# Performance work log

Measured on AMD Instinct MI355X. Metric: run time of the kernel, lower is better.

The kernel has to match this reference:

```python
import jax, jax.numpy as jnp
import numpy as np

B, S, D, H, MLP = 2, 2048, 1024, 16, 4096
DH = D // H
EPS_LN = 1e-6
KERNEL_EPS = 1e-3  # fast_attention generalized kernel_epsilon


def layer_norm(x, scale, bias):
    m = jnp.mean(x, axis=-1, keepdims=True)
    v = jnp.mean(jnp.square(x - m), axis=-1, keepdims=True)
    return (x - m) * jax.lax.rsqrt(v + EPS_LN) * scale + bias


def performer_causal_attention(q, k, v):
    """FAVOR+ generalized attention (deterministic relu features), causal.

    q,k,v: [B,S,H,DH]. phi(x) = relu(x) + eps. Linear-time via prefix sums:
      out_i = phi(q_i) . cumsum_j<=i phi(k_j) v_j^T / (phi(q_i) . cumsum phi(k_j))
    """
    phi_q = jax.nn.relu(q) + KERNEL_EPS          # [B,S,H,M]
    phi_k = jax.nn.relu(k) + KERNEL_EPS          # [B,S,H,M]
    kv = jnp.cumsum(jnp.einsum('bshm,bshd->bshmd', phi_k, v), axis=1)  # [B,S,H,M,DH]
    num = jnp.einsum('bshm,bshmd->bshd', phi_q, kv)
    den = jnp.einsum('bshm,bshm->bsh', phi_q, jnp.cumsum(phi_k, axis=1))
    return num / den[..., None]


def setup_inputs() -> dict:
    key = jax.random.key(0)
    ks = jax.random.split(key, 7)
    def w(k, shape, scale):
        return jax.random.normal(k, shape, jnp.float32) * scale
    s_in = 1.0 / np.sqrt(D)
    return {
        'inputs': jax.random.normal(ks[0], (B, S, D), jnp.float32),
        'ln1_scale': jnp.ones((D,), jnp.float32),
        'ln1_bias': jnp.zeros((D,), jnp.float32),
        'wq': w(ks[1], (D, H, DH), s_in),
        'wk': w(ks[2], (D, H, DH), s_in),
        'wv': w(ks[3], (D, H, DH), s_in),
        'wo': w(ks[4], (H, DH, D), s_in),
        'ln2_scale': jnp.ones((D,), jnp.float32),
        'ln2_bias': jnp.zeros((D,), jnp.float32),
        'w1': w(ks[5], (D, MLP), s_in),
        'b1': jnp.zeros((MLP,), jnp.float32),
        'w2': w(ks[6], (MLP, D), 1.0 / np.sqrt(MLP)),
        'b2': jnp.zeros((D,), jnp.float32),
    }


def reference(inputs, ln1_scale, ln1_bias, wq, wk, wv, wo,
              ln2_scale, ln2_bias, w1, b1, w2, b2):
    # pre-LN self-attention (Performer FAVOR+ generalized, causal)
    x = layer_norm(inputs, ln1_scale, ln1_bias)
    q = jnp.einsum('bsd,dhm->bshm', x, wq)
    k = jnp.einsum('bsd,dhm->bshm', x, wk)
    v = jnp.einsum('bsd,dhm->bshm', x, wv)
    attn = performer_causal_attention(q, k, v)          # [B,S,H,DH]
    attn_out = jnp.einsum('bshm,hmd->bsd', attn, wo)    # output projection
    x = attn_out + inputs                               # residual
    # pre-LN MLP block
    y = layer_norm(x, ln2_scale, ln2_bias)
    y = jax.nn.gelu(y @ w1 + b1) @ w2 + b2
    return x + y
```

## Files before the change

### kernel.cpp

```cpp
#include <hip/hip_runtime.h>
#include <math.h>
#include <stdint.h>

typedef __bf16 bf16;
typedef bf16  bf16x8 __attribute__((ext_vector_type(8)));
typedef float f32x4  __attribute__((ext_vector_type(4)));

constexpr int Bb  = 2;
constexpr int Ss  = 2048;
constexpr int Dd  = 1024;
constexpr int Hh  = 16;
constexpr int DHh = 64;
constexpr int MLPd = 4096;
constexpr int ROWS = Bb * Ss;
constexpr int NC  = Ss / 64;
constexpr int BH  = Bb * Hh;
constexpr float EPS_LN = 1e-6f;
constexpr float KEPS   = 1e-3f;

__device__ __forceinline__ void async_copy16(const bf16* g, bf16* l) {
    __builtin_amdgcn_global_load_lds(
        (__attribute__((address_space(1))) void*)g,
        (__attribute__((address_space(3))) void*)l,
        16, 0, 0);
}

__device__ __forceinline__ int swz64(int row, int col) {
    return row * 64 + (((col >> 3) ^ row) & 7) * 8 + (col & 7);
}

__global__ __launch_bounds__(256) void ln_kernel(const float* __restrict__ x,
                                                 const float* __restrict__ scale,
                                                 const float* __restrict__ bias,
                                                 bf16* __restrict__ out)
{
    const int row = blockIdx.x;
    const float* xr = x + (size_t)row * Dd;
    float vals[4];
    float sum = 0.f, sumsq = 0.f;
#pragma unroll
    for (int i = 0; i < 4; i++) {
        float v = xr[threadIdx.x + 256 * i];
        vals[i] = v;
        sum += v;
        sumsq += v * v;
    }
#pragma unroll
    for (int off = 32; off > 0; off >>= 1) {
        sum   += __shfl_down(sum, off);
        sumsq += __shfl_down(sumsq, off);
    }
    __shared__ float ssum[4], ssq[4];
    const int wave = threadIdx.x >> 6;
    if ((threadIdx.x & 63) == 0) { ssum[wave] = sum; ssq[wave] = sumsq; }
    __syncthreads();
    const float tot   = ssum[0] + ssum[1] + ssum[2] + ssum[3];
    const float totsq = ssq[0] + ssq[1] + ssq[2] + ssq[3];
    const float mean = tot * (1.f / Dd);
    const float var  = totsq * (1.f / Dd) - mean * mean;
    const float r = rsqrtf(var + EPS_LN);
    bf16* orow = out + (size_t)row * Dd;
#pragma unroll
    for (int i = 0; i < 4; i++) {
        const int c = threadIdx.x + 256 * i;
        orow[c] = (bf16)((vals[i] - mean) * r * scale[c] + bias[c]);
    }
}

__global__ __launch_bounds__(256) void convert_T(const float* __restrict__ in,
                                                 bf16* __restrict__ out,
                                                 int K, int N)
{
    __shared__ float tile[32][33];
    const int k0 = blockIdx.y * 32, n0 = blockIdx.x * 32;
    const int tx = threadIdx.x & 31, ty = threadIdx.x >> 5;
#pragma unroll
    for (int i = 0; i < 32; i += 8)
        tile[ty + i][tx] = in[(size_t)(k0 + ty + i) * N + n0 + tx];
    __syncthreads();
#pragma unroll
    for (int i = 0; i < 32; i += 8)
        out[(size_t)(n0 + ty + i) * K + k0 + tx] = (bf16)tile[tx][ty + i];
}

__global__ __launch_bounds__(256) void convert_T4(const float* __restrict__ s0,
                                                  const float* __restrict__ s1,
                                                  const float* __restrict__ s2,
                                                  const float* __restrict__ s3,
                                                  bf16* __restrict__ d0,
                                                  bf16* __restrict__ d1,
                                                  bf16* __restrict__ d2,
                                                  bf16* __restrict__ d3)
{
    const float* in  = (blockIdx.z == 0) ? s0 : (blockIdx.z == 1) ? s1
                     : (blockIdx.z == 2) ? s2 : s3;
    bf16* out        = (blockIdx.z == 0) ? d0 : (blockIdx.z == 1) ? d1
                     : (blockIdx.z == 2) ? d2 : d3;
    __shared__ float tile[32][33];
    const int k0 = blockIdx.y * 32, n0 = blockIdx.x * 32;
    const int tx = threadIdx.x & 31, ty = threadIdx.x >> 5;
#pragma unroll
    for (int i = 0; i < 32; i += 8)
        tile[ty + i][tx] = in[(size_t)(k0 + ty + i) * 1024 + n0 + tx];
    __syncthreads();
#pragma unroll
    for (int i = 0; i < 32; i += 8)
        out[(size_t)(n0 + ty + i) * 1024 + k0 + tx] = (bf16)tile[tx][ty + i];
}

enum { EP_QKV = 0, EP_NONE = 1, EP_RES = 2, EP_GELU = 3, EP_BIAS_RES = 4 };

template <int TN, int BK, int MODE>
__global__ __launch_bounds__(256) void mfma_gemm(const bf16* __restrict__ A,
                                                 const bf16* __restrict__ BT,
                                                 void* __restrict__ Cout,
                                                 int M, int N, int K,
                                                 const float* __restrict__ bias,
                                                 const float* __restrict__ res,
                                                 bf16* __restrict__ out2,
                                                 bf16* __restrict__ out3)
{
    constexpr int WCT = TN / 2;
    constexpr int NJ  = TN / 32;
    constexpr int NS  = BK / 32;
    constexpr int CPR = BK / 8;
    constexpr int RPI = 2048 / BK;
    __shared__ bf16 As[128 * BK];
    __shared__ bf16 Bs[TN * BK];
    const int t = threadIdx.x;
    const int wave = t >> 6, lane = t & 63;
    const int row0 = blockIdx.y * 128, col0 = blockIdx.x * TN;
    const int wr = wave >> 1, wc = wave & 1;

    const int srow = t / CPR;
    const int gch  = (t % CPR) ^ (srow & 7);
    const int sdst = t * 8;

    const int m = lane & 15, quad = lane >> 4;
    const int mx7 = m & 7;

    f32x4 acc[4][NJ] = {};

    for (int k0 = 0; k0 < K; k0 += BK) {
        __syncthreads();
#pragma unroll
        for (int i = 0; i < 128 / RPI; i++) {
            const int r = i * RPI + srow;
            async_copy16(A + (size_t)(row0 + r) * K + k0 + gch * 8,
                         &As[i * 2048 + sdst]);
        }
#pragma unroll
        for (int i = 0; i < TN / RPI; i++) {
            const int r = i * RPI + srow;
            async_copy16(BT + (size_t)(col0 + r) * K + k0 + gch * 8,
                         &Bs[i * 2048 + sdst]);
        }
        __syncthreads();

#pragma unroll
        for (int s = 0; s < NS; s++) {
            const int pco = ((s * 4 + quad) ^ mx7) * 8;
            bf16x8 aF[4], bF[NJ];
#pragma unroll
            for (int i = 0; i < 4; i++)
                aF[i] = *(const bf16x8*)&As[(wr * 64 + i * 16 + m) * BK + pco];
#pragma unroll
            for (int j = 0; j < NJ; j++)
                bF[j] = *(const bf16x8*)&Bs[(wc * WCT + j * 16 + m) * BK + pco];
#pragma unroll
            for (int i = 0; i < 4; i++)
#pragma unroll
                for (int j = 0; j < NJ; j++)
                    acc[i][j] = __builtin_amdgcn_mfma_f32_16x16x32_bf16(
                        aF[i], bF[j], acc[i][j], 0, 0, 0);
        }
    }

    bf16* qkv_dst = nullptr;
    int col_base = col0;
    bool do_phi = false;
    if constexpr (MODE == EP_QKV) {
        const int third = col0 >> 10;
        qkv_dst = (third == 0) ? (bf16*)Cout : (third == 1) ? out2 : out3;
        col_base = col0 & 1023;
        do_phi = (third < 2);
    }

#pragma unroll
    for (int i = 0; i < 4; i++) {
#pragma unroll
        for (int j = 0; j < NJ; j++) {
#pragma unroll
            for (int r = 0; r < 4; r++) {
                const int row = row0 + wr * 64 + i * 16 + quad * 4 + r;
                const int col = col0 + wc * WCT + j * 16 + m;
                float val = acc[i][j][r];
                if constexpr (MODE == EP_QKV) {
                    const int lc = col_base + wc * WCT + j * 16 + m;
                    if (do_phi) val = fmaxf(val, 0.f) + KEPS;
                    qkv_dst[(size_t)row * 1024 + lc] = (bf16)val;
                } else if constexpr (MODE == EP_NONE) {
                    ((bf16*)Cout)[(size_t)row * N + col] = (bf16)val;
                } else if constexpr (MODE == EP_RES) {
                    ((float*)Cout)[(size_t)row * N + col] = val + res[(size_t)row * N + col];
                } else if constexpr (MODE == EP_GELU) {
                    val += bias[col];
                    const float u = 0.7978845608028654f * (val + 0.044715f * val * val * val);
                    const float e = __expf(2.f * u);
                    val = val * (1.f - 1.f / (e + 1.f));
                    ((bf16*)Cout)[(size_t)row * N + col] = (bf16)val;
                } else {
                    val += bias[col] + res[(size_t)row * N + col];
                    ((float*)Cout)[(size_t)row * N + col] = val;
                }
            }
        }
    }
}

__global__ __launch_bounds__(256) void chunk_kv_kernel(const bf16* __restrict__ phik,
                                                       const bf16* __restrict__ v,
                                                       float* __restrict__ kvs,
                                                       float* __restrict__ ksums)
{
    const int c = blockIdx.x, bh = blockIdx.y;
    const int b = bh >> 4, h = bh & 15;
    __shared__ bf16 Kt[64 * 64];
    __shared__ bf16 Vt[64 * 64];
    const int t = threadIdx.x;
    const int wave = t >> 6, lane = t & 63;
    const int m16 = lane & 15, quad = lane >> 4;
    const int wr = wave >> 1, wc = wave & 1;
    const int f = t & 63, s4 = t >> 6;

#pragma unroll
    for (int i = 0; i < 16; i++) {
        const int s = s4 + 4 * i;
        const size_t g = ((size_t)((b * Ss + c * 64 + s) * Hh + h)) * DHh + f;
        Kt[swz64(f, s)] = phik[g];
        Vt[swz64(f, s)] = v[g];
    }
    __syncthreads();

    f32x4 acc[2][2] = {};
#pragma unroll
    for (int ks = 0; ks < 2; ks++) {
        bf16x8 aF[2], bF[2];
#pragma unroll
        for (int i = 0; i < 2; i++)
            aF[i] = *(const bf16x8*)&Kt[swz64(wr * 32 + i * 16 + m16, ks * 32 + quad * 8)];
#pragma unroll
        for (int j = 0; j < 2; j++)
            bF[j] = *(const bf16x8*)&Vt[swz64(wc * 32 + j * 16 + m16, ks * 32 + quad * 8)];
#pragma unroll
        for (int i = 0; i < 2; i++)
#pragma unroll
            for (int j = 0; j < 2; j++)
                acc[i][j] = __builtin_amdgcn_mfma_f32_16x16x32_bf16(
                    aF[i], bF[j], acc[i][j], 0, 0, 0);
    }

    const size_t base = ((size_t)bh * NC + c) * 4096;
#pragma unroll
    for (int i = 0; i < 2; i++)
#pragma unroll
        for (int j = 0; j < 2; j++)
#pragma unroll
            for (int r = 0; r < 4; r++) {
                const int mrow = wr * 32 + i * 16 + quad * 4 + r;
                const int dcol = wc * 32 + j * 16 + m16;
                kvs[base + mrow * 64 + dcol] = acc[i][j][r];
            }

    if (t < 64) {
        float s_ = 0.f;
#pragma unroll
        for (int p = 0; p < 8; p++) {
            bf16x8 k8 = *(const bf16x8*)&Kt[t * 64 + p * 8];
#pragma unroll
            for (int e = 0; e < 8; e++) s_ += (float)k8[e];
        }
        ksums[((size_t)bh * NC + c) * 64 + t] = s_;
    }
}

__global__ __launch_bounds__(256) void scan_kernel(float* __restrict__ kvs,
                                                   float* __restrict__ ksums)
{
    const int e  = blockIdx.x * 256 + threadIdx.x;
    const int bh = blockIdx.y;
    float run = 0.f;
#pragma unroll 4
    for (int c = 0; c < NC; c++) {
        const size_t idx = ((size_t)bh * NC + c) * 4096 + e;
        const float val = kvs[idx];
        kvs[idx] = run;
        run += val;
    }
    if (blockIdx.x == 0 && threadIdx.x < 64) {
        float r = 0.f;
        for (int c = 0; c < NC; c++) {
            const size_t idx = ((size_t)bh * NC + c) * 64 + threadIdx.x;
            const float val = ksums[idx];
            ksums[idx] = r;
            r += val;
        }
    }
}

__global__ __launch_bounds__(256) void attn_out_kernel(const bf16* __restrict__ phiq,
                                                       const bf16* __restrict__ phik,
                                                       const bf16* __restrict__ v,
                                                       const float* __restrict__ kvs,
                                                       const float* __restrict__ ksums,
                                                       bf16* __restrict__ attn)
{
    const int c = blockIdx.x, bh = blockIdx.y;
    const int b = bh >> 4, h = bh & 15;
    __shared__ bf16 Qs [64 * 64];
    __shared__ bf16 KVb[64 * 64];
    __shared__ bf16 Sm [64 * 64];
    __shared__ bf16 KVt[64 * 64];
    __shared__ float ksm[64], den[64];
    const int t = threadIdx.x;
    const int wave = t >> 6, lane = t & 63;
    const int m16 = lane & 15, quad = lane >> 4;
    const int wr = wave >> 1, wc = wave & 1;
    const int f = t & 63, s4 = t >> 6;

#pragma unroll
    for (int i = 0; i < 16; i++) {
        const int s = s4 + 4 * i;
        const size_t g = ((size_t)((b * Ss + c * 64 + s) * Hh + h)) * DHh + f;
        Qs [swz64(s, f)] = phiq[g];
        KVb[swz64(s, f)] = phik[g];
    }
    if (t < 64) ksm[t] = ksums[((size_t)bh * NC + c) * 64 + t];
    __syncthreads();

    f32x4 sacc[2][2] = {};
#pragma unroll
    for (int ks = 0; ks < 2; ks++) {
        bf16x8 aF[2], bF[2];
#pragma unroll
        for (int i = 0; i < 2; i++)
            aF[i] = *(const bf16x8*)&Qs [swz64(wr * 32 + i * 16 + m16, ks * 32 + quad * 8)];
#pragma unroll
        for (int j = 0; j < 2; j++)
            bF[j] = *(const bf16x8*)&KVb[swz64(wc * 32 + j * 16 + m16, ks * 32 + quad * 8)];
#pragma unroll
        for (int i = 0; i < 2; i++)
#pragma unroll
            for (int j = 0; j < 2; j++)
                sacc[i][j] = __builtin_amdgcn_mfma_f32_16x16x32_bf16(
                    aF[i], bF[j], sacc[i][j], 0, 0, 0);
    }
#pragma unroll
    for (int i = 0; i < 2; i++)
#pragma unroll
        for (int j = 0; j < 2; j++)
#pragma unroll
            for (int r = 0; r < 4; r++) {
                const int row = wr * 32 + i * 16 + quad * 4 + r;
                const int col = wc * 32 + j * 16 + m16;
                Sm[swz64(row, col)] = (bf16)((col <= row) ? sacc[i][j][r] : 0.f);
            }
    __syncthreads();

#pragma unroll
    for (int i = 0; i < 16; i++) {
        const int s = s4 + 4 * i;
        const size_t g = ((size_t)((b * Ss + c * 64 + s) * Hh + h)) * DHh + f;
        KVb[swz64(f, s)] = v[g];
    }
    {
        const size_t base = ((size_t)bh * NC + c) * 4096;
#pragma unroll
        for (int i = 0; i < 16; i++) {
            const int e = t + 256 * i;
            KVt[swz64(e & 63, e >> 6)] = (bf16)kvs[base + e];
        }
    }
    __syncthreads();

    if (t < 64) {
        float d_ = 0.f;
#pragma unroll
        for (int p = 0; p < 8; p++) {
            const int gc = (p ^ (t & 7)) * 8;
            bf16x8 q8 = *(const bf16x8*)&Qs[t * 64 + p * 8];
            bf16x8 s8 = *(const bf16x8*)&Sm[t * 64 + p * 8];
#pragma unroll
            for (int e = 0; e < 8; e++)
                d_ += (float)q8[e] * ksm[gc + e] + (float)s8[e];
        }
        den[t] = d_;
    }

    f32x4 oacc[2][2] = {};
#pragma unroll
    for (int ks = 0; ks < 2; ks++) {
        bf16x8 aF[2], bF[2];
#pragma unroll
        for (int i = 0; i < 2; i++)
            aF[i] = *(const bf16x8*)&Sm [swz64(wr * 32 + i * 16 + m16, ks * 32 + quad * 8)];
#pragma unroll
        for (int j = 0; j < 2; j++)
            bF[j] = *(const bf16x8*)&KVb[swz64(wc * 32 + j * 16 + m16, ks * 32 + quad * 8)];
#pragma unroll
        for (int i = 0; i < 2; i++)
#pragma unroll
            for (int j = 0; j < 2; j++)
                oacc[i][j] = __builtin_amdgcn_mfma_f32_16x16x32_bf16(
                    aF[i], bF[j], oacc[i][j], 0, 0, 0);
    }
#pragma unroll
    for (int ks = 0; ks < 2; ks++) {
        bf16x8 aF[2], bF[2];
#pragma unroll
        for (int i = 0; i < 2; i++)
            aF[i] = *(const bf16x8*)&Qs [swz64(wr * 32 + i * 16 + m16, ks * 32 + quad * 8)];
#pragma unroll
        for (int j = 0; j < 2; j++)
            bF[j] = *(const bf16x8*)&KVt[swz64(wc * 32 + j * 16 + m16, ks * 32 + quad * 8)];
#pragma unroll
        for (int i = 0; i < 2; i++)
#pragma unroll
            for (int j = 0; j < 2; j++)
                oacc[i][j] = __builtin_amdgcn_mfma_f32_16x16x32_bf16(
                    aF[i], bF[j], oacc[i][j], 0, 0, 0);
    }
    __syncthreads();

#pragma unroll
    for (int i = 0; i < 2; i++) {
#pragma unroll
        for (int r = 0; r < 4; r++) {
            const int row = wr * 32 + i * 16 + quad * 4 + r;
            const float dinv = 1.f / den[row];
#pragma unroll
            for (int j = 0; j < 2; j++) {
                const int col = wc * 32 + j * 16 + m16;
                attn[((size_t)((b * Ss + c * 64 + row) * Hh + h)) * DHh + col] =
                    (bf16)(oacc[i][j][r] * dinv);
            }
        }
    }
}

extern "C" void kernel_launch(void* const* d_in, const int* in_sizes, int n_in,
                              void* d_out, int out_size, void* d_ws, size_t ws_size,
                              hipStream_t stream)
{
    const float* inputs    = (const float*)d_in[0];
    const float* ln1_scale = (const float*)d_in[1];
    const float* ln1_bias  = (const float*)d_in[2];
    const float* wq        = (const float*)d_in[3];
    const float* wk        = (const float*)d_in[4];
    const float* wv        = (const float*)d_in[5];
    const float* wo        = (const float*)d_in[6];
    const float* ln2_scale = (const float*)d_in[7];
    const float* ln2_bias  = (const float*)d_in[8];
    const float* w1        = (const float*)d_in[9];
    const float* b1        = (const float*)d_in[10];
    const float* w2        = (const float*)d_in[11];
    const float* b2        = (const float*)d_in[12];
    float* out = (float*)d_out;

    char* ws = (char*)d_ws;
    bf16*  xln   = (bf16*)ws;
    bf16*  q     = (bf16*)(ws + (8ull  << 20));
    bf16*  k     = (bf16*)(ws + (16ull << 20));
    bf16*  v     = (bf16*)(ws + (24ull << 20));
    float* kvs   = (float*)(ws + (32ull << 20));
    float* x2    = (float*)(ws + (48ull << 20));
    float* ksums = (float*)(ws + (64ull << 20));
    bf16*  wqT   = (bf16*)(ws + (64ull << 20) + (1ull << 18));
    bf16*  wkT   = wqT + 1024 * 1024;
    bf16*  wvT   = wkT + 1024 * 1024;
    bf16*  woT   = wvT + 1024 * 1024;
    bf16*  w1T   = woT + 1024 * 1024;
    bf16*  w2T   = w1T + 4096 * 1024;
    bf16*  attn  = xln;
    bf16*  yln   = q;
    bf16*  hbuf  = k;

    convert_T4<<<dim3(32, 32, 4), 256, 0, stream>>>(wq, wk, wv, wo, wqT, wkT, wvT, woT);
    convert_T<<<dim3(4096 / 32, 1024 / 32), 256, 0, stream>>>(w1, w1T, 1024, 4096);
    convert_T<<<dim3(1024 / 32, 4096 / 32), 256, 0, stream>>>(w2, w2T, 4096, 1024);

    ln_kernel<<<ROWS, 256, 0, stream>>>(inputs, ln1_scale, ln1_bias, xln);

    mfma_gemm<128, 64, EP_QKV><<<dim3(3072 / 128, ROWS / 128), 256, 0, stream>>>(
        xln, wqT, q, ROWS, 3072, 1024, nullptr, nullptr, k, v);

    {
        dim3 gridA(NC, BH);
        chunk_kv_kernel<<<gridA, 256, 0, stream>>>(k, v, kvs, ksums);
        scan_kernel<<<dim3(4096 / 256, BH), 256, 0, stream>>>(kvs, ksums);
        attn_out_kernel<<<gridA, 256, 0, stream>>>(q, k, v, kvs, ksums, attn);
    }

    mfma_gemm<64, 128, EP_RES><<<dim3(1024 / 64, ROWS / 128), 256, 0, stream>>>(
        attn, woT, x2, ROWS, 1024, 1024, nullptr, inputs, nullptr, nullptr);

    ln_kernel<<<ROWS, 256, 0, stream>>>(x2, ln2_scale, ln2_bias, yln);

    mfma_gemm<128, 64, EP_GELU><<<dim3(MLPd / 128, ROWS / 128), 256, 0, stream>>>(
        yln, w1T, hbuf, ROWS, MLPd, 1024, b1, nullptr, nullptr, nullptr);
    mfma_gemm<64, 128, EP_BIAS_RES><<<dim3(1024 / 64, ROWS / 128), 256, 0, stream>>>(
        hbuf, w2T, out, ROWS, 1024, MLPd, b2, x2, nullptr, nullptr);
}
```

Baseline: 310.3 us.

## Specialize GEMM dims at compile time and store chunk KV states in bf16

The GEMM kernel now takes N and K as template parameters and advances precomputed global pointers each K step, which cuts per-iteration address arithmetic. Separately, the per-chunk KV state buffer moves from fp32 to bf16, halving traffic in chunk_kv, scan and attn_out. The scan still accumulates in fp32, but it writes bf16 prefixes, so precision is reduced slightly.

```diff
diff --git a/kernel.cpp b/kernel.cpp
--- a/kernel.cpp
+++ b/kernel.cpp
@@ -110,11 +110,10 @@
 
 enum { EP_QKV = 0, EP_NONE = 1, EP_RES = 2, EP_GELU = 3, EP_BIAS_RES = 4 };
 
-template <int TN, int BK, int MODE>
+template <int TN, int BK, int NDIM, int KDIM, int MODE>
 __global__ __launch_bounds__(256) void mfma_gemm(const bf16* __restrict__ A,
                                                  const bf16* __restrict__ BT,
                                                  void* __restrict__ Cout,
-                                                 int M, int N, int K,
                                                  const float* __restrict__ bias,
                                                  const float* __restrict__ res,
                                                  bf16* __restrict__ out2,
@@ -136,25 +135,22 @@
     const int gch  = (t % CPR) ^ (srow & 7);
     const int sdst = t * 8;
 
+    const bf16* gA = A  + (size_t)(row0 + srow) * KDIM + gch * 8;
+    const bf16* gB = BT + (size_t)(col0 + srow) * KDIM + gch * 8;
+
     const int m = lane & 15, quad = lane >> 4;
     const int mx7 = m & 7;
 
     f32x4 acc[4][NJ] = {};
 
-    for (int k0 = 0; k0 < K; k0 += BK) {
+    for (int k0 = 0; k0 < KDIM; k0 += BK) {
         __syncthreads();
 #pragma unroll
-        for (int i = 0; i < 128 / RPI; i++) {
-            const int r = i * RPI + srow;
-            async_copy16(A + (size_t)(row0 + r) * K + k0 + gch * 8,
-                         &As[i * 2048 + sdst]);
-        }
-#pragma unroll
-        for (int i = 0; i < TN / RPI; i++) {
-            const int r = i * RPI + srow;
-            async_copy16(BT + (size_t)(col0 + r) * K + k0 + gch * 8,
-                         &Bs[i * 2048 + sdst]);
-        }
+        for (int i = 0; i < 128 / RPI; i++)
+            async_copy16(gA + (size_t)i * RPI * KDIM, &As[i * 2048 + sdst]);
+#pragma unroll
+        for (int i = 0; i < TN / RPI; i++)
+            async_copy16(gB + (size_t)i * RPI * KDIM, &Bs[i * 2048 + sdst]);
         __syncthreads();
 
 #pragma unroll
@@ -174,6 +170,8 @@
                     acc[i][j] = __builtin_amdgcn_mfma_f32_16x16x32_bf16(
                         aF[i], bF[j], acc[i][j], 0, 0, 0);
         }
+        gA += BK;
+        gB += BK;
     }
 
     bf16* qkv_dst = nullptr;
@@ -200,18 +198,18 @@
                     if (do_phi) val = fmaxf(val, 0.f) + KEPS;
                     qkv_dst[(size_t)row * 1024 + lc] = (bf16)val;
                 } else if constexpr (MODE == EP_NONE) {
-                    ((bf16*)Cout)[(size_t)row * N + col] = (bf16)val;
+                    ((bf16*)Cout)[(size_t)row * NDIM + col] = (bf16)val;
                 } else if constexpr (MODE == EP_RES) {
-                    ((float*)Cout)[(size_t)row * N + col] = val + res[(size_t)row * N + col];
+                    ((float*)Cout)[(size_t)row * NDIM + col] = val + res[(size_t)row * NDIM + col];
                 } else if constexpr (MODE == EP_GELU) {
                     val += bias[col];
                     const float u = 0.7978845608028654f * (val + 0.044715f * val * val * val);
                     const float e = __expf(2.f * u);
                     val = val * (1.f - 1.f / (e + 1.f));
-                    ((bf16*)Cout)[(size_t)row * N + col] = (bf16)val;
+                    ((bf16*)Cout)[(size_t)row * NDIM + col] = (bf16)val;
                 } else {
-                    val += bias[col] + res[(size_t)row * N + col];
-                    ((float*)Cout)[(size_t)row * N + col] = val;
+                    val += bias[col] + res[(size_t)row * NDIM + col];
+                    ((float*)Cout)[(size_t)row * NDIM + col] = val;
                 }
             }
         }
@@ -220,7 +218,7 @@
 
 __global__ __launch_bounds__(256) void chunk_kv_kernel(const bf16* __restrict__ phik,
                                                        const bf16* __restrict__ v,
-                                                       float* __restrict__ kvs,
+                                                       bf16* __restrict__ kvs,
                                                        float* __restrict__ ksums)
 {
     const int c = blockIdx.x, bh = blockIdx.y;
@@ -269,7 +267,7 @@
             for (int r = 0; r < 4; r++) {
                 const int mrow = wr * 32 + i * 16 + quad * 4 + r;
                 const int dcol = wc * 32 + j * 16 + m16;
-                kvs[base + mrow * 64 + dcol] = acc[i][j][r];
+                kvs[base + mrow * 64 + dcol] = (bf16)acc[i][j][r];
             }
 
     if (t < 64) {
@@ -284,7 +282,7 @@
     }
 }
 
-__global__ __launch_bounds__(256) void scan_kernel(float* __restrict__ kvs,
+__global__ __launch_bounds__(256) void scan_kernel(bf16* __restrict__ kvs,
                                                    float* __restrict__ ksums)
 {
     const int e  = blockIdx.x * 256 + threadIdx.x;
@@ -293,8 +291,8 @@
 #pragma unroll 4
     for (int c = 0; c < NC; c++) {
         const size_t idx = ((size_t)bh * NC + c) * 4096 + e;
-        const float val = kvs[idx];
-        kvs[idx] = run;
+        const float val = (float)kvs[idx];
+        kvs[idx] = (bf16)run;
         run += val;
     }
     if (blockIdx.x == 0 && threadIdx.x < 64) {
@@ -311,7 +309,7 @@
 __global__ __launch_bounds__(256) void attn_out_kernel(const bf16* __restrict__ phiq,
                                                        const bf16* __restrict__ phik,
                                                        const bf16* __restrict__ v,
-                                                       const float* __restrict__ kvs,
+                                                       const bf16* __restrict__ kvs,
                                                        const float* __restrict__ ksums,
                                                        bf16* __restrict__ attn)
 {
@@ -378,7 +376,7 @@
 #pragma unroll
         for (int i = 0; i < 16; i++) {
             const int e = t + 256 * i;
-            KVt[swz64(e & 63, e >> 6)] = (bf16)kvs[base + e];
+            KVt[swz64(e & 63, e >> 6)] = kvs[base + e];
         }
     }
     __syncthreads();
@@ -472,7 +470,7 @@
     bf16*  q     = (bf16*)(ws + (8ull  << 20));
     bf16*  k     = (bf16*)(ws + (16ull << 20));
     bf16*  v     = (bf16*)(ws + (24ull << 20));
-    float* kvs   = (float*)(ws + (32ull << 20));
+    bf16*  kvs   = (bf16*)(ws + (32ull << 20));
     float* x2    = (float*)(ws + (48ull << 20));
     float* ksums = (float*)(ws + (64ull << 20));
     bf16*  wqT   = (bf16*)(ws + (64ull << 20) + (1ull << 18));
@@ -491,8 +489,8 @@
 
     ln_kernel<<<ROWS, 256, 0, stream>>>(inputs, ln1_scale, ln1_bias, xln);
 
-    mfma_gemm<128, 64, EP_QKV><<<dim3(3072 / 128, ROWS / 128), 256, 0, stream>>>(
-        xln, wqT, q, ROWS, 3072, 1024, nullptr, nullptr, k, v);
+    mfma_gemm<128, 64, 3072, 1024, EP_QKV><<<dim3(3072 / 128, ROWS / 128), 256, 0, stream>>>(
+        xln, wqT, q, nullptr, nullptr, k, v);
 
     {
         dim3 gridA(NC, BH);
@@ -501,13 +499,13 @@
         attn_out_kernel<<<gridA, 256, 0, stream>>>(q, k, v, kvs, ksums, attn);
     }
 
-    mfma_gemm<64, 128, EP_RES><<<dim3(1024 / 64, ROWS / 128), 256, 0, stream>>>(
-        attn, woT, x2, ROWS, 1024, 1024, nullptr, inputs, nullptr, nullptr);
+    mfma_gemm<64, 128, 1024, 1024, EP_RES><<<dim3(1024 / 64, ROWS / 128), 256, 0, stream>>>(
+        attn, woT, x2, nullptr, inputs, nullptr, nullptr);
 
     ln_kernel<<<ROWS, 256, 0, stream>>>(x2, ln2_scale, ln2_bias, yln);
 
-    mfma_gemm<128, 64, EP_GELU><<<dim3(MLPd / 128, ROWS / 128), 256, 0, stream>>>(
-        yln, w1T, hbuf, ROWS, MLPd, 1024, b1, nullptr, nullptr, nullptr);
-    mfma_gemm<64, 128, EP_BIAS_RES><<<dim3(1024 / 64, ROWS / 128), 256, 0, stream>>>(
-        hbuf, w2T, out, ROWS, 1024, MLPd, b2, x2, nullptr, nullptr);
-}
+    mfma_gemm<128, 64, 4096, 1024, EP_GELU><<<dim3(MLPd / 128, ROWS / 128), 256, 0, stream>>>(
+        yln, w1T, hbuf, b1, nullptr, nullptr, nullptr);
+    mfma_gemm<64, 128, 1024, 4096, EP_BIAS_RES><<<dim3(1024 / 64, ROWS / 128), 256, 0, stream>>>(
+        hbuf, w2T, out, b2, x2, nullptr, nullptr);
+}
```

Result: no change. 313.3 us (+1.0%).
